# Performance work log

Measured on AMD Instinct MI355X. Metric: run time of the kernel, lower is better.

Reference implementation:

```python
import jax, jax.numpy as jnp
import numpy as np

B, S, D, H = 2, 2048, 2048, 16
HD = D // H  # head_dim = 128


def rotate_half(x):
    x1, x2 = x[..., : x.shape[-1] // 2], x[..., x.shape[-1] // 2 :]
    return jnp.concatenate((-x2, x1), axis=-1)


def setup_inputs() -> dict:
    key = jax.random.key(0)
    ks = jax.random.split(key, 6)
    x = jax.random.normal(ks[0], (B, S, D), dtype=jnp.float32)
    # RoPE cos/sin tables, shape [B, S, head_dim]
    inv_freq = 1.0 / (10000.0 ** (np.arange(0, HD, 2, dtype=np.float32) / HD))
    t = np.arange(S, dtype=np.float32)
    freqs = np.outer(t, inv_freq)                      # [S, HD/2]
    emb = np.concatenate([freqs, freqs], axis=-1)      # [S, HD]
    cos = jnp.broadcast_to(jnp.cos(emb), (B, S, HD)).astype(jnp.float32)
    sin = jnp.broadcast_to(jnp.sin(emb), (B, S, HD)).astype(jnp.float32)
    attn_mask = jnp.zeros((B, S), dtype=jnp.float32)   # additive 2D mask
    scale = 0.02
    wq = jax.random.normal(ks[1], (D, D), dtype=jnp.float32) * scale
    wk = jax.random.normal(ks[2], (D, D), dtype=jnp.float32) * scale
    wv = jax.random.normal(ks[3], (D, D), dtype=jnp.float32) * scale
    wo = jax.random.normal(ks[4], (D, D), dtype=jnp.float32) * scale
    return {"x": x, "cos": cos, "sin": sin, "attn_mask": attn_mask,
            "wq": wq, "wk": wk, "wv": wv, "wo": wo}


def reference(x, cos, sin, attn_mask, wq, wk, wv, wo):
    b, s, d = x.shape
    # fused-style QKV projections (nn.Linear: y = x @ W.T), reshape to [b,h,s,hd]
    def proj(w):
        return jnp.einsum('bsd,ed->bse', x, w).reshape(b, s, H, HD).transpose(0, 2, 1, 3)
    q, k, v = proj(wq), proj(wk), proj(wv)
    # RoPE: cos/sin [b,s,hd] -> broadcast over heads
    c = cos[:, None, :, :]
    sn = sin[:, None, :, :]
    q = q * c + rotate_half(q) * sn
    k = k * c + rotate_half(k) * sn
    # SDPA with additive 2D mask -> [b,1,1,s]
    scores = jnp.einsum('bhqd,bhkd->bhqk', q, k) / jnp.sqrt(jnp.float32(HD))
    scores = scores + attn_mask[:, None, None, :]
    attn = jax.nn.softmax(scores, axis=-1)
    out = jnp.einsum('bhqk,bhkd->bhqd', attn, v)
    out = out.transpose(0, 2, 1, 3).reshape(b, s, d)
    return jnp.einsum('bsd,ed->bse', out, wo)
```

## Files before the change

kernel.cpp:

```cpp
#include <hip/hip_runtime.h>

#define B_  2
#define S_  2048
#define D_  2048
#define H_  16
#define HD_ 128

typedef float  f32x4  __attribute__((ext_vector_type(4)));
typedef float  f32x16 __attribute__((ext_vector_type(16)));
typedef __bf16 bf16x8 __attribute__((ext_vector_type(8)));
typedef unsigned int u32;

__device__ __forceinline__ void gl16(const void* g, void* l) {
  __builtin_amdgcn_global_load_lds(
      (const __attribute__((address_space(1))) unsigned int*)g,
      (__attribute__((address_space(3))) unsigned int*)l, 16, 0, 0);
}

__device__ __forceinline__ ushort f2bf(float f) {
  union { float f; unsigned u; } v; v.f = f;
  unsigned r = v.u + 0x7FFFu + ((v.u >> 16) & 1u);
  return (ushort)(r >> 16);
}
__device__ __forceinline__ float bf2f(ushort b) {
  union { unsigned u; float f; } v; v.u = ((unsigned)b) << 16;
  return v.f;
}
__device__ __forceinline__ f32x4 fzero() {
  f32x4 v; v[0] = 0.f; v[1] = 0.f; v[2] = 0.f; v[3] = 0.f; return v;
}
__device__ __forceinline__ float exp2x(float x) {
  return __builtin_amdgcn_exp2f(x);
}

__global__ void cvt4(const float* __restrict__ s, ushort* __restrict__ d, int n4) {
  int i = blockIdx.x * blockDim.x + threadIdx.x;
  if (i >= n4) return;
  float4 v = ((const float4*)s)[i];
  ushort4 o = make_ushort4(f2bf(v.x), f2bf(v.y), f2bf(v.z), f2bf(v.w));
  ((ushort4*)d)[i] = o;
}

template<int MODE>
__global__ __launch_bounds__(256, 2)
void gemm_bt(const ushort* __restrict__ A, const ushort* __restrict__ Bp,
             void* __restrict__ Cp, int M, int N, int K)
{
  __shared__ __align__(16) ushort lds[2][2][128 * 32];
  const int tid  = threadIdx.x;
  const int wave = tid >> 6, lane = tid & 63;
  const int qt = lane >> 4, ln = lane & 15;
  const int wr = wave >> 1, wc = wave & 1;
  const int bm = blockIdx.x * 128, bn = blockIdx.y * 128;

  f32x4 acc[4][4];
#pragma unroll
  for (int a = 0; a < 4; ++a)
#pragma unroll
    for (int b = 0; b < 4; ++b) acc[a][b] = fzero();

  auto stage = [&](int buf, int kt) {
#pragma unroll
    for (int it = 0; it < 2; ++it) {
      int c = it * 256 + tid;
      int row = c >> 2, ch = c & 3;
      int chs = ch ^ ((row >> 1) & 3);
      gl16(A  + (size_t)(bm + row) * K + kt + chs * 8,
           (void*)&lds[buf][0][(it * 256 + wave * 64) * 8]);
      gl16(Bp + (size_t)(bn + row) * K + kt + chs * 8,
           (void*)&lds[buf][1][(it * 256 + wave * 64) * 8]);
    }
  };

  const int nk = K >> 5;
  stage(0, 0);
  int cur = 0;
  for (int kt = 0; kt < nk; ++kt) {
    __syncthreads();
    if (kt + 1 < nk) stage(cur ^ 1, (kt + 1) << 5);
    bf16x8 af[4], bfr[4];
#pragma unroll
    for (int mf = 0; mf < 4; ++mf) {
      int row = wr * 64 + mf * 16 + ln;
      int sl = qt ^ ((row >> 1) & 3);
      af[mf] = *(const bf16x8*)&lds[cur][0][row * 32 + sl * 8];
    }
#pragma unroll
    for (int nf = 0; nf < 4; ++nf) {
      int row = wc * 64 + nf * 16 + ln;
      int sl = qt ^ ((row >> 1) & 3);
      bfr[nf] = *(const bf16x8*)&lds[cur][1][row * 32 + sl * 8];
    }
#pragma unroll
    for (int mf = 0; mf < 4; ++mf)
#pragma unroll
      for (int nf = 0; nf < 4; ++nf)
        acc[mf][nf] = __builtin_amdgcn_mfma_f32_16x16x32_bf16(
            af[mf], bfr[nf], acc[mf][nf], 0, 0, 0);
    cur ^= 1;
  }

#pragma unroll
  for (int mf = 0; mf < 4; ++mf)
#pragma unroll
    for (int nf = 0; nf < 4; ++nf) {
      int m0 = bm + wr * 64 + mf * 16 + qt * 4;
      int n  = bn + wc * 64 + nf * 16 + ln;
#pragma unroll
      for (int i = 0; i < 4; ++i) {
        int m = m0 + i;
        if (MODE == 0) {
          ((float*)Cp)[(size_t)m * N + n] = acc[mf][nf][i];
        } else {
          int b = m >> 11, s = m & 2047;
          int h = n >> 7,  d = n & 127;
          if (MODE == 1)
            ((ushort*)Cp)[(((size_t)b * H_ + h) * S_ + s) * HD_ + d] = f2bf(acc[mf][nf][i]);
          else
            ((ushort*)Cp)[(((size_t)b * H_ + h) * HD_ + d) * S_ + s] = f2bf(acc[mf][nf][i]);
        }
      }
    }
}

__global__ void rope_qk(ushort* __restrict__ Q, ushort* __restrict__ Kt,
                        const float* __restrict__ cs, const float* __restrict__ sn)
{
  int t = blockIdx.x * 256 + threadIdx.x;
  int d  = t & 63;
  int rr = t >> 6;
  int isk = rr >> 16;
  int bhs = rr & 65535;
  int s = bhs & 2047;
  int b = bhs >> 15;
  ushort* P = isk ? Kt : Q;
  size_t ro = (size_t)bhs * HD_;
  float q0 = bf2f(P[ro + d]), q1 = bf2f(P[ro + d + 64]);
  size_t ci = ((size_t)b * S_ + s) * HD_ + d;
  float c0 = cs[ci], s0 = sn[ci], c1 = cs[ci + 64], s1 = sn[ci + 64];
  P[ro + d]      = f2bf(q0 * c0 - q1 * s0);
  P[ro + d + 64] = f2bf(q1 * c1 + q0 * s1);
}

__global__ __launch_bounds__(256, 2)
void flash(const ushort* __restrict__ Q, const ushort* __restrict__ Kk,
           const ushort* __restrict__ VT, const float* __restrict__ mask,
           ushort* __restrict__ O)
{
  __shared__ __align__(16) ushort kt_s[2][64 * 128];
  __shared__ __align__(16) ushort vt_s[128 * 64];

  const int tid = threadIdx.x;
  const int wave = tid >> 6, lane = tid & 63;
  const int ln32 = lane & 31, hi = lane >> 5;
  const int bh = blockIdx.x, b = bh >> 4, h = bh & 15;
  const size_t base  = (size_t)bh * S_ * HD_;
  const size_t baseT = (size_t)bh * HD_ * S_;
  const int q0 = blockIdx.y * 128 + wave * 32;
  const float L2E = 1.4426950408889634f;
  const float scale2 = 0.08838834764831845f * L2E;

  bf16x8 qf[8];
  {
    const ushort* qrow = Q + base + (size_t)(q0 + ln32) * HD_;
#pragma unroll
    for (int hd = 0; hd < 8; ++hd)
      qf[hd] = *(const bf16x8*)(qrow + hd * 16 + hi * 8);
  }

  f32x16 accO[4];
#pragma unroll
  for (int dblk = 0; dblk < 4; ++dblk)
#pragma unroll
    for (int i = 0; i < 16; ++i) accO[dblk][i] = 0.f;
  float mrun = -1e30f;
  float lrun = 0.f;

  auto stageK = [&](int buf, int k0) {
#pragma unroll
    for (int it = 0; it < 4; ++it) {
      int c = it * 256 + tid;
      int row = c >> 4, ch = c & 15;
      int chs = ch ^ (row & 7);
      gl16(Kk + base + (size_t)(k0 + row) * HD_ + chs * 8,
           (void*)&kt_s[buf][(it * 256 + wave * 64) * 8]);
    }
  };
  auto stageV = [&](int k0) {
#pragma unroll
    for (int it = 0; it < 4; ++it) {
      int c = it * 256 + tid;
      int d = c >> 3, ch = c & 7;
      int chs = ch ^ (d & 7);
      gl16(VT + baseT + (size_t)d * S_ + k0 + chs * 8,
           (void*)&vt_s[(it * 256 + wave * 64) * 8]);
    }
  };

  stageK(0, 0);
  stageV(0);
  int cur = 0;
  for (int k0 = 0; k0 < S_; k0 += 64) {
    __syncthreads();
    if (k0 + 64 < S_) stageK(cur ^ 1, k0 + 64);

    f32x16 sc[2];
    __builtin_amdgcn_s_setprio(1);
#pragma unroll
    for (int kblk = 0; kblk < 2; ++kblk) {
      f32x16 a;
#pragma unroll
      for (int i = 0; i < 16; ++i) a[i] = 0.f;
      int row = kblk * 32 + ln32;
#pragma unroll
      for (int hd = 0; hd < 8; ++hd) {
        int sl = (hd * 2 + hi) ^ (row & 7);
        bf16x8 kf = *(const bf16x8*)&kt_s[cur][row * 128 + sl * 8];
        a = __builtin_amdgcn_mfma_f32_32x32x16_bf16(kf, qf[hd], a, 0, 0, 0);
      }
      sc[kblk] = a;
    }
    __builtin_amdgcn_s_setprio(0);

    float sv[2][16];
#pragma unroll
    for (int kblk = 0; kblk < 2; ++kblk)
#pragma unroll
      for (int g = 0; g < 4; ++g) {
        float4 mk = *(const float4*)&mask[(size_t)b * S_ + k0 + kblk * 32 + g * 8 + hi * 4];
        sv[kblk][g * 4 + 0] = sc[kblk][g * 4 + 0] * scale2 + mk.x * L2E;
        sv[kblk][g * 4 + 1] = sc[kblk][g * 4 + 1] * scale2 + mk.y * L2E;
        sv[kblk][g * 4 + 2] = sc[kblk][g * 4 + 2] * scale2 + mk.z * L2E;
        sv[kblk][g * 4 + 3] = sc[kblk][g * 4 + 3] * scale2 + mk.w * L2E;
      }

    float m = sv[0][0];
#pragma unroll
    for (int kblk = 0; kblk < 2; ++kblk)
#pragma unroll
      for (int i = 0; i < 16; ++i) m = fmaxf(m, sv[kblk][i]);
    m = fmaxf(m, __shfl_xor(m, 32));

    if (__any(m > mrun + 8.f)) {
      float mn = fmaxf(mrun, m);
      float fsc = exp2x(mrun - mn);
      mrun = mn;
      lrun *= fsc;
      float fq[16];
#pragma unroll
      for (int g = 0; g < 4; ++g)
#pragma unroll
        for (int j = 0; j < 4; ++j)
          fq[g * 4 + j] = __shfl(fsc, j + 8 * g + 4 * hi);
#pragma unroll
      for (int dblk = 0; dblk < 4; ++dblk)
#pragma unroll
        for (int i = 0; i < 16; ++i) accO[dblk][i] *= fq[i];
    }

    float tsum = 0.f;
    ushort pb[2][16];
#pragma unroll
    for (int kblk = 0; kblk < 2; ++kblk)
#pragma unroll
      for (int i = 0; i < 16; ++i) {
        float p = exp2x(sv[kblk][i] - mrun);
        __bf16 pq = (__bf16)p;
        union { __bf16 b; ushort s; } cc; cc.b = pq;
        pb[kblk][i] = cc.s;
        tsum += (float)pq;
      }
    lrun += tsum;

    bf16x8 pa[4];
#pragma unroll
    for (int kblk = 0; kblk < 2; ++kblk) {
      u32 pk0[4], pk1[4];
#pragma unroll
      for (int t = 0; t < 4; ++t) {
        pk0[t] = (u32)pb[kblk][4 * t]     | ((u32)pb[kblk][4 * t + 1] << 16);
        pk1[t] = (u32)pb[kblk][4 * t + 2] | ((u32)pb[kblk][4 * t + 3] << 16);
      }
#pragma unroll
      for (int c = 0; c < 2; ++c) {
        u32 a0 = pk0[2 * c],     a1 = pk1[2 * c];
        u32 b0 = pk0[2 * c + 1], b1 = pk1[2 * c + 1];
        u32 s0 = hi ? a0 : b0,   s1 = hi ? a1 : b1;
        u32 r0 = (u32)__shfl_xor((int)s0, 32);
        u32 r1 = (u32)__shfl_xor((int)s1, 32);
        u32 o0 = hi ? b0 : a0,   o1 = hi ? b1 : a1;
        u32 w[4];
        w[0] = hi ? r0 : o0;  w[1] = hi ? r1 : o1;
        w[2] = hi ? o0 : r0;  w[3] = hi ? o1 : r1;
        pa[kblk * 2 + c] = *(bf16x8*)w;
      }
    }

    __builtin_amdgcn_s_setprio(1);
#pragma unroll
    for (int kk = 0; kk < 4; ++kk)
#pragma unroll
      for (int dblk = 0; dblk < 4; ++dblk) {
        int d = dblk * 32 + ln32;
        int sl = (kk * 2 + hi) ^ (d & 7);
        bf16x8 vf = *(const bf16x8*)&vt_s[d * 64 + sl * 8];
        accO[dblk] = __builtin_amdgcn_mfma_f32_32x32x16_bf16(pa[kk], vf, accO[dblk], 0, 0, 0);
      }
    __builtin_amdgcn_s_setprio(0);

    __syncthreads();
    if (k0 + 64 < S_) stageV(k0 + 64);
    cur ^= 1;
  }

  lrun += __shfl_xor(lrun, 32);
  float inv_own = 1.f / lrun;
  float invv[16];
#pragma unroll
  for (int g = 0; g < 4; ++g)
#pragma unroll
    for (int j = 0; j < 4; ++j)
      invv[g * 4 + j] = __shfl(inv_own, j + 8 * g + 4 * hi);
#pragma unroll
  for (int dblk = 0; dblk < 4; ++dblk)
#pragma unroll
    for (int g = 0; g < 4; ++g)
#pragma unroll
      for (int j = 0; j < 4; ++j) {
        int q = j + 8 * g + 4 * hi;
        size_t idx = ((size_t)b * S_ + q0 + q) * D_ + h * HD_ + dblk * 32 + ln32;
        O[idx] = f2bf(accO[dblk][g * 4 + j] * invv[g * 4 + j]);
      }
}

extern "C" void kernel_launch(void* const* d_in, const int* in_sizes, int n_in,
                              void* d_out, int out_size, void* d_ws, size_t ws_size,
                              hipStream_t stream)
{
  if (n_in != 8) return;
  if (in_sizes[0] != 8388608) return;
  if (in_sizes[3] != 4096)    return;
  if (out_size != 8388608) return;
  if (ws_size < (size_t)96 * 1024 * 1024) return;

  const float* x    = (const float*)d_in[0];
  const float* cosb = (const float*)d_in[1];
  const float* sinb = (const float*)d_in[2];
  const float* mask = (const float*)d_in[3];
  const float* wq   = (const float*)d_in[4];
  const float* wk   = (const float*)d_in[5];
  const float* wv   = (const float*)d_in[6];
  const float* wo   = (const float*)d_in[7];

  char* ws = (char*)d_ws;
  ushort* xb  = (ushort*)(ws);
  ushort* wqb = (ushort*)(ws + 16777216);
  ushort* wkb = (ushort*)(ws + 25165824);
  ushort* wvb = (ushort*)(ws + 33554432);
  ushort* wob = (ushort*)(ws + 41943040);
  ushort* Qb  = (ushort*)(ws + 50331648);
  ushort* Kb  = (ushort*)(ws + 67108864);
  ushort* VTb = (ushort*)(ws + 83886080);
  ushort* AOb = xb;

  cvt4<<<8192, 256, 0, stream>>>(x,  xb,  2097152);
  cvt4<<<4096, 256, 0, stream>>>(wq, wqb, 1048576);
  cvt4<<<4096, 256, 0, stream>>>(wk, wkb, 1048576);
  cvt4<<<4096, 256, 0, stream>>>(wv, wvb, 1048576);
  cvt4<<<4096, 256, 0, stream>>>(wo, wob, 1048576);

  dim3 gg(32, 16);
  gemm_bt<1><<<gg, 256, 0, stream>>>(xb, wqb, Qb,  4096, 2048, 2048);
  gemm_bt<1><<<gg, 256, 0, stream>>>(xb, wkb, Kb,  4096, 2048, 2048);
  gemm_bt<3><<<gg, 256, 0, stream>>>(xb, wvb, VTb, 4096, 2048, 2048);

  rope_qk<<<32768, 256, 0, stream>>>(Qb, Kb, cosb, sinb);

  flash<<<dim3(32, 16), 256, 0, stream>>>(Qb, Kb, VTb, mask, AOb);

  gemm_bt<0><<<gg, 256, 0, stream>>>(AOb, wob, d_out, 4096, 2048, 2048);
}
```

Before: 303.4 us.

## Fuse conversions and QKV GEMMs into single launches; switch LDS swizzle to rotation

The five fp32-to-bf16 conversion launches become one kernel that writes x and all four weights contiguously into the workspace. The three Q/K/V projection GEMMs become one N=6144 GEMM whose epilogue routes each column block to Q, K or transposed V. The flash kernel's K and V LDS swizzle changes from XOR to an additive rotation scheme to alter bank-conflict behaviour. Fewer launches and a larger grid aim to cut launch overhead and tail effects, but the epilogue gains branching and the new swizzle may conflict differently.

```diff
diff --git a/kernel.cpp b/kernel.cpp
--- a/kernel.cpp
+++ b/kernel.cpp
@@ -33,12 +33,21 @@
   return __builtin_amdgcn_exp2f(x);
 }
 
-__global__ void cvt4(const float* __restrict__ s, ushort* __restrict__ d, int n4) {
+__global__ void cvt_all(const float* __restrict__ x,  const float* __restrict__ wq,
+                        const float* __restrict__ wk, const float* __restrict__ wv,
+                        const float* __restrict__ wo, ushort* __restrict__ dst)
+{
   int i = blockIdx.x * blockDim.x + threadIdx.x;
-  if (i >= n4) return;
-  float4 v = ((const float4*)s)[i];
-  ushort4 o = make_ushort4(f2bf(v.x), f2bf(v.y), f2bf(v.z), f2bf(v.w));
-  ((ushort4*)d)[i] = o;
+  if (i >= 6291456) return;
+  const float* s;
+  int t = i - 2097152;
+  if (t < 0)             { s = x;  t = i; }
+  else if (t < 1048576)  { s = wq; }
+  else if (t < 2097152)  { s = wk; t -= 1048576; }
+  else if (t < 3145728)  { s = wv; t -= 2097152; }
+  else                   { s = wo; t -= 3145728; }
+  float4 v = ((const float4*)s)[t];
+  ((ushort4*)dst)[i] = make_ushort4(f2bf(v.x), f2bf(v.y), f2bf(v.z), f2bf(v.w));
 }
 
 template<int MODE>
@@ -113,11 +122,14 @@
           ((float*)Cp)[(size_t)m * N + n] = acc[mf][nf][i];
         } else {
           int b = m >> 11, s = m & 2047;
-          int h = n >> 7,  d = n & 127;
-          if (MODE == 1)
-            ((ushort*)Cp)[(((size_t)b * H_ + h) * S_ + s) * HD_ + d] = f2bf(acc[mf][nf][i]);
-          else
-            ((ushort*)Cp)[(((size_t)b * H_ + h) * HD_ + d) * S_ + s] = f2bf(acc[mf][nf][i]);
+          int which = n >> 11;
+          int nn = n & 2047;
+          int h = nn >> 7, d = nn & 127;
+          size_t off = (size_t)which * 8388608;
+          size_t idx = (which == 2)
+              ? (((size_t)b * H_ + h) * HD_ + d) * S_ + s
+              : (((size_t)b * H_ + h) * S_ + s) * HD_ + d;
+          ((ushort*)Cp)[off + idx] = f2bf(acc[mf][nf][i]);
         }
       }
     }
@@ -180,8 +192,8 @@
 #pragma unroll
     for (int it = 0; it < 4; ++it) {
       int c = it * 256 + tid;
-      int row = c >> 4, ch = c & 15;
-      int chs = ch ^ (row & 7);
+      int row = c >> 4, sl = c & 15;
+      int chs = (sl - (row >> 1)) & 15;
       gl16(Kk + base + (size_t)(k0 + row) * HD_ + chs * 8,
            (void*)&kt_s[buf][(it * 256 + wave * 64) * 8]);
     }
@@ -190,8 +202,8 @@
 #pragma unroll
     for (int it = 0; it < 4; ++it) {
       int c = it * 256 + tid;
-      int d = c >> 3, ch = c & 7;
-      int chs = ch ^ (d & 7);
+      int d = c >> 3, sl = c & 7;
+      int chs = (sl - (d >> 2)) & 7;
       gl16(VT + baseT + (size_t)d * S_ + k0 + chs * 8,
            (void*)&vt_s[(it * 256 + wave * 64) * 8]);
     }
@@ -214,7 +226,7 @@
       int row = kblk * 32 + ln32;
 #pragma unroll
       for (int hd = 0; hd < 8; ++hd) {
-        int sl = (hd * 2 + hi) ^ (row & 7);
+        int sl = (hd * 2 + hi + (row >> 1)) & 15;
         bf16x8 kf = *(const bf16x8*)&kt_s[cur][row * 128 + sl * 8];
         a = __builtin_amdgcn_mfma_f32_32x32x16_bf16(kf, qf[hd], a, 0, 0, 0);
       }
@@ -302,7 +314,7 @@
 #pragma unroll
       for (int dblk = 0; dblk < 4; ++dblk) {
         int d = dblk * 32 + ln32;
-        int sl = (kk * 2 + hi) ^ (d & 7);
+        int sl = (kk * 2 + hi + (d >> 2)) & 7;
         bf16x8 vf = *(const bf16x8*)&vt_s[d * 64 + sl * 8];
         accO[dblk] = __builtin_amdgcn_mfma_f32_32x32x16_bf16(pa[kk], vf, accO[dblk], 0, 0, 0);
       }
@@ -353,30 +365,21 @@
   const float* wo   = (const float*)d_in[7];
 
   char* ws = (char*)d_ws;
-  ushort* xb  = (ushort*)(ws);
-  ushort* wqb = (ushort*)(ws + 16777216);
-  ushort* wkb = (ushort*)(ws + 25165824);
-  ushort* wvb = (ushort*)(ws + 33554432);
-  ushort* wob = (ushort*)(ws + 41943040);
-  ushort* Qb  = (ushort*)(ws + 50331648);
-  ushort* Kb  = (ushort*)(ws + 67108864);
-  ushort* VTb = (ushort*)(ws + 83886080);
-  ushort* AOb = xb;
-
-  cvt4<<<8192, 256, 0, stream>>>(x,  xb,  2097152);
-  cvt4<<<4096, 256, 0, stream>>>(wq, wqb, 1048576);
-  cvt4<<<4096, 256, 0, stream>>>(wk, wkb, 1048576);
-  cvt4<<<4096, 256, 0, stream>>>(wv, wvb, 1048576);
-  cvt4<<<4096, 256, 0, stream>>>(wo, wob, 1048576);
-
-  dim3 gg(32, 16);
-  gemm_bt<1><<<gg, 256, 0, stream>>>(xb, wqb, Qb,  4096, 2048, 2048);
-  gemm_bt<1><<<gg, 256, 0, stream>>>(xb, wkb, Kb,  4096, 2048, 2048);
-  gemm_bt<3><<<gg, 256, 0, stream>>>(xb, wvb, VTb, 4096, 2048, 2048);
+  ushort* xb   = (ushort*)(ws);
+  ushort* wqkv = (ushort*)(ws + 16777216);
+  ushort* wob  = (ushort*)(ws + 41943040);
+  ushort* Qb   = (ushort*)(ws + 50331648);
+  ushort* Kb   = (ushort*)(ws + 67108864);
+  ushort* VTb  = (ushort*)(ws + 83886080);
+  ushort* AOb  = xb;
+
+  cvt_all<<<24576, 256, 0, stream>>>(x, wq, wk, wv, wo, xb);
+
+  gemm_bt<4><<<dim3(32, 48), 256, 0, stream>>>(xb, wqkv, Qb, 4096, 6144, 2048);
 
   rope_qk<<<32768, 256, 0, stream>>>(Qb, Kb, cosb, sinb);
 
   flash<<<dim3(32, 16), 256, 0, stream>>>(Qb, Kb, VTb, mask, AOb);
 
-  gemm_bt<0><<<gg, 256, 0, stream>>>(AOb, wob, d_out, 4096, 2048, 2048);
-}
+  gemm_bt<0><<<dim3(32, 16), 256, 0, stream>>>(AOb, wob, d_out, 4096, 2048, 2048);
+}
```

Result: no change. 306.3 us (+1.0%).
